# Kernel optimization log

Hardware: AMD Instinct MI355X
Metric: run time of the kernel (lower is better)

## Reference

```python
import jax, jax.numpy as jnp
import numpy as np

N_NODES = 50000
N_EDGES = 800000
IN_CH = 64
OUT_CH = 64


def setup_inputs() -> dict:
    key = jax.random.key(0)
    ks = jax.random.split(key, 20)
    inp = {
        'x': jax.random.normal(ks[0], (N_NODES, IN_CH), dtype=jnp.float32),
        'edge_index': jax.random.randint(ks[1], (2, N_EDGES), 0, N_NODES, dtype=jnp.int64),
        'edge_weight': jax.random.uniform(ks[2], (N_EDGES,), dtype=jnp.float32),
    }
    i = 3
    for g in ('z', 'r', 'h'):
        inp[f'Wx_{g}'] = 0.1 * jax.random.normal(ks[i], (2, IN_CH, OUT_CH), dtype=jnp.float32); i += 1
        inp[f'bx_{g}'] = 0.1 * jax.random.normal(ks[i], (OUT_CH,), dtype=jnp.float32); i += 1
        inp[f'Wh_{g}'] = 0.1 * jax.random.normal(ks[i], (2, OUT_CH, OUT_CH), dtype=jnp.float32); i += 1
        inp[f'bh_{g}'] = 0.1 * jax.random.normal(ks[i], (OUT_CH,), dtype=jnp.float32); i += 1
    inp['lin_W'] = 0.1 * jax.random.normal(ks[i], (OUT_CH, 1), dtype=jnp.float32); i += 1
    inp['lin_b'] = jnp.zeros((1,), dtype=jnp.float32)
    return inp


def _cheb_norm(edge_index, edge_weight, n_nodes):
    # sym-normalized scaled Laplacian with lambda_max=2: L_hat = -D^{-1/2} A D^{-1/2}
    src, dst = edge_index[0], edge_index[1]
    deg = jax.ops.segment_sum(edge_weight, src, num_segments=n_nodes)
    dinv = jnp.where(deg > 0, jax.lax.rsqrt(jnp.where(deg > 0, deg, 1.0)), 0.0)
    norm = -dinv[src] * edge_weight * dinv[dst]
    return src, dst, norm


def _cheb_conv(x, src, dst, norm, W, b, n_nodes):
    # K=2: out = x @ W0 + (L_hat x) @ W1 + b
    out = x @ W[0]
    tx1 = jax.ops.segment_sum(norm[:, None] * x[src], dst, num_segments=n_nodes)
    out = out + tx1 @ W[1]
    return out + b


def reference(x, edge_index, edge_weight,
              Wx_z, bx_z, Wh_z, bh_z,
              Wx_r, bx_r, Wh_r, bh_r,
              Wx_h, bx_h, Wh_h, bh_h,
              lin_W, lin_b):
    n = x.shape[0]
    src, dst, norm = _cheb_norm(edge_index, edge_weight, n)
    H = jnp.zeros((n, OUT_CH), dtype=x.dtype)  # GConvGRU initial hidden state
    Z = jax.nn.sigmoid(_cheb_conv(x, src, dst, norm, Wx_z, bx_z, n)
                       + _cheb_conv(H, src, dst, norm, Wh_z, bh_z, n))
    R = jax.nn.sigmoid(_cheb_conv(x, src, dst, norm, Wx_r, bx_r, n)
                       + _cheb_conv(H, src, dst, norm, Wh_r, bh_r, n))
    H_tilde = jnp.tanh(_cheb_conv(x, src, dst, norm, Wx_h, bx_h, n)
                       + _cheb_conv(H * R, src, dst, norm, Wh_h, bh_h, n))
    H = Z * H + (1.0 - Z) * H_tilde
    h = jax.nn.relu(H)
    return h @ lin_W + lin_b
```

## Files before the change

### kernel.cpp

```cpp
#include <hip/hip_runtime.h>
#include <hip/hip_bf16.h>

#define NN 50000
#define NE 800000
#define NB 196
#define BCAPD 4608
#define BCAPS 4608
#define EPT 4
#define BIN_BLOCKS ((NE + 256*EPT - 1) / (256*EPT))

typedef __attribute__((ext_vector_type(4))) float f4;
typedef __attribute__((ext_vector_type(4))) float f32x4;
typedef __attribute__((ext_vector_type(8))) short bf16x8;
typedef __attribute__((ext_vector_type(4))) unsigned int u32x4;
typedef __attribute__((ext_vector_type(2))) unsigned int u32x2;

#define OFF_TX1  0
#define OFF_BIND 0
#define OFF_BINS (NB*BCAPD*2)
#define OFF_DINV (OFF_BINS + NB*BCAPS)
#define OFF_CNT  (OFF_DINV + NN)
#define OFF_GC   (OFF_CNT + NN)
#define OFF_BIAS (OFF_GC + 2*NB)
#define OFF_WT   (OFF_BIAS + 196)
#define OFF_XB   (OFF_WT + 8192)
#define OFF_EREC (OFF_XB + NN*32)

__device__ __forceinline__ unsigned int bpack(float a, float b) {
    return ((__float_as_uint(a) + 0x8000u) >> 16)
         | ((__float_as_uint(b) + 0x8000u) & 0xffff0000u);
}

__global__ __launch_bounds__(256) void k_prep(const float* __restrict__ x,
                       const float* __restrict__ Wxz, const float* __restrict__ bxz,
                       const float* __restrict__ bhz,
                       const float* __restrict__ Wxh, const float* __restrict__ bxh,
                       const float* __restrict__ bhh,
                       const float* __restrict__ linW, const float* __restrict__ linb,
                       float* __restrict__ bias, unsigned short* __restrict__ wt,
                       unsigned int* __restrict__ xb, int* __restrict__ gc) {
    int idx = blockIdx.x * 256 + threadIdx.x;
    if (idx < NN * 16) {
        f4 v = *(const f4*)&x[(size_t)idx * 4];
        u32x2 p = { bpack(v[0], v[1]), bpack(v[2], v[3]) };
        *(u32x2*)&xb[(size_t)idx * 2] = p;
    }
    if (idx < 2 * 64 * 128) {
        int g = idx >> 13;
        int c = (idx >> 7) & 63;
        int k = idx & 127;
        const float* W = g ? Wxh : Wxz;
        float v = (k < 64) ? W[k * 64 + c] : W[4096 + (k - 64) * 64 + c];
        wt[idx] = (unsigned short)((__float_as_uint(v) + 0x8000u) >> 16);
    }
    if (idx < 64) {
        bias[idx]       = bxz[idx] + bhz[idx];
        bias[64 + idx]  = bxh[idx] + bhh[idx];
        bias[128 + idx] = linW[idx];
    }
    if (idx == 64) bias[192] = linb[0];
    if (idx < 2 * NB) gc[idx] = 0;
}

__global__ __launch_bounds__(256) void k_bin(const int* __restrict__ ei,
                                             const float* __restrict__ ew,
                                             int2* __restrict__ binD,
                                             unsigned int* __restrict__ binS,
                                             int* __restrict__ gcD, int* __restrict__ gcS) {
    __shared__ int hD[NB], hS[NB], bD[NB], bS[NB];
    int t = threadIdx.x;
    for (int b = t; b < NB; b += 256) { hD[b] = 0; hS[b] = 0; }
    __syncthreads();

    int e0 = blockIdx.x * (256 * EPT);
    unsigned int sa[EPT];
    float wv[EPT];
    int sd[EPT], ss[EPT];
#pragma unroll
    for (int i = 0; i < EPT; i++) {
        int e = e0 + i * 256 + t;
        sd[i] = -1; ss[i] = -1; sa[i] = 0; wv[i] = 0.f;
        if (e < NE) {
            int s = ei[e];
            int d = ei[NE + e];
            wv[i] = ew[e];
            int bind = d >> 8;
            sa[i] = (unsigned int)s | ((unsigned int)(d & 255) << 16)
                  | ((unsigned int)bind << 24);
            sd[i] = atomicAdd(&hD[bind], 1);
            ss[i] = atomicAdd(&hS[s >> 8], 1);
        }
    }
    __syncthreads();
    for (int b = t; b < NB; b += 256) {
        bD[b] = atomicAdd(&gcD[b], hD[b]);
        bS[b] = atomicAdd(&gcS[b], hS[b]);
    }
    __syncthreads();
#pragma unroll
    for (int i = 0; i < EPT; i++) {
        if (sd[i] < 0) continue;
        unsigned int a = sa[i];
        int bind = a >> 24;
        int src  = a & 0xffff;
        int pD = bD[bind] + sd[i];
        if (pD < BCAPD)
            binD[bind * BCAPD + pD] = make_int2((int)(a & 0xffffff), __float_as_int(wv[i]));
        int bins = src >> 8;
        int pS = bS[bins] + ss[i];
        if (pS < BCAPS)
            binS[bins * BCAPS + pS] = ((unsigned int)(src & 255) << 16)
                                    | ((__float_as_uint(wv[i]) + 0x8000u) >> 16);
    }
}

__global__ __launch_bounds__(1024) void k_split(const int2* __restrict__ binD,
                                                const unsigned int* __restrict__ binS,
                                                const int* __restrict__ gc,
                                                unsigned int* __restrict__ erec, int cap,
                                                int* __restrict__ cnt,
                                                float* __restrict__ dinv) {
    __shared__ unsigned int sh[256];
    int t = threadIdx.x;
    if (blockIdx.x < NB) {
        int bin = blockIdx.x;
        int* lcnt = (int*)sh;
        if (t < 256) lcnt[t] = 0;
        __syncthreads();
        int m = gc[bin]; if (m > BCAPD) m = BCAPD;
        const int2* bp = binD + (size_t)bin * BCAPD;
        for (int j = t; j < m; j += 1024) {
            int2 r = bp[j];
            int dlo = (r.x >> 16) & 255;
            int src = r.x & 0xffff;
            int slot = atomicAdd(&lcnt[dlo], 1);
            if (slot < cap) {
                unsigned int wr = (__float_as_uint(__int_as_float(r.y)) + 0x8000u) >> 16;
                erec[(size_t)(bin * 256 + dlo) * cap + slot] = ((unsigned int)src << 16) | wr;
            }
        }
        __syncthreads();
        if (t < 256) {
            int idx = bin * 256 + t;
            if (idx < NN) cnt[idx] = lcnt[t];
        }
    } else {
        int bin = blockIdx.x - NB;
        float* acc = (float*)sh;
        if (t < 256) acc[t] = 0.f;
        __syncthreads();
        int m = gc[NB + bin]; if (m > BCAPS) m = BCAPS;
        const unsigned int* bp = binS + (size_t)bin * BCAPS;
        for (int j = t; j < m; j += 1024) {
            unsigned int r = bp[j];
            atomicAdd(&acc[r >> 16], __uint_as_float((r & 0xffffu) << 16));
        }
        __syncthreads();
        if (t < 256) {
            int idx = bin * 256 + t;
            if (idx < NN) {
                float d = acc[t];
                dinv[idx] = (d > 0.f) ? (1.f / sqrtf(d)) : 0.f;
            }
        }
    }
}

__global__ __launch_bounds__(256) void k_gather(const unsigned int* __restrict__ xb,
                                                const int* __restrict__ cnt,
                                                const float* __restrict__ dinv,
                                                const unsigned int* __restrict__ erec,
                                                int cap, unsigned int* __restrict__ tx1) {
    int w = (blockIdx.x * 256 + threadIdx.x) >> 6;
    if (w >= NN) return;
    int lane = threadIdx.x & 63;
    int g  = lane >> 3;
    int c8 = (lane & 7) * 4;
    int kn = cnt[w];
    if (kn > cap) kn = cap;
    const unsigned int* bp = erec + (size_t)w * cap;

    f4 p0 = {0.f,0.f,0.f,0.f}, p1 = {0.f,0.f,0.f,0.f};
    f4 q0 = {0.f,0.f,0.f,0.f}, q1 = {0.f,0.f,0.f,0.f};
    int j = 0;
    for (; j + 15 < kn; j += 16) {
        unsigned int r0 = bp[j + g];
        unsigned int r1 = bp[j + 8 + g];
        int s0 = r0 >> 16, s1 = r1 >> 16;
        float n0 = dinv[s0] * __uint_as_float((r0 & 0xffffu) << 16);
        float n1 = dinv[s1] * __uint_as_float((r1 & 0xffffu) << 16);
        u32x4 v0 = *(const u32x4*)&xb[(size_t)s0 * 32 + c8];
        u32x4 v1 = *(const u32x4*)&xb[(size_t)s1 * 32 + c8];
#pragma unroll
        for (int q = 0; q < 2; q++) {
            p0[2*q]   = fmaf(n0, __uint_as_float(v0[q] << 16), p0[2*q]);
            p0[2*q+1] = fmaf(n0, __uint_as_float(v0[q] & 0xffff0000u), p0[2*q+1]);
            p1[2*q]   = fmaf(n0, __uint_as_float(v0[2+q] << 16), p1[2*q]);
            p1[2*q+1] = fmaf(n0, __uint_as_float(v0[2+q] & 0xffff0000u), p1[2*q+1]);
            q0[2*q]   = fmaf(n1, __uint_as_float(v1[q] << 16), q0[2*q]);
            q0[2*q+1] = fmaf(n1, __uint_as_float(v1[q] & 0xffff0000u), q0[2*q+1]);
            q1[2*q]   = fmaf(n1, __uint_as_float(v1[2+q] << 16), q1[2*q]);
            q1[2*q+1] = fmaf(n1, __uint_as_float(v1[2+q] & 0xffff0000u), q1[2*q+1]);
        }
    }
    for (; j + 7 < kn; j += 8) {
        unsigned int r0 = bp[j + g];
        int s0 = r0 >> 16;
        float n0 = dinv[s0] * __uint_as_float((r0 & 0xffffu) << 16);
        u32x4 v0 = *(const u32x4*)&xb[(size_t)s0 * 32 + c8];
#pragma unroll
        for (int q = 0; q < 2; q++) {
            p0[2*q]   = fmaf(n0, __uint_as_float(v0[q] << 16), p0[2*q]);
            p0[2*q+1] = fmaf(n0, __uint_as_float(v0[q] & 0xffff0000u), p0[2*q+1]);
            p1[2*q]   = fmaf(n0, __uint_as_float(v0[2+q] << 16), p1[2*q]);
            p1[2*q+1] = fmaf(n0, __uint_as_float(v0[2+q] & 0xffff0000u), p1[2*q+1]);
        }
    }
    int rem = kn - j;
    if (g < rem) {
        unsigned int r0 = bp[j + g];
        int s0 = r0 >> 16;
        float n0 = dinv[s0] * __uint_as_float((r0 & 0xffffu) << 16);
        u32x4 v0 = *(const u32x4*)&xb[(size_t)s0 * 32 + c8];
#pragma unroll
        for (int q = 0; q < 2; q++) {
            p0[2*q]   = fmaf(n0, __uint_as_float(v0[q] << 16), p0[2*q]);
            p0[2*q+1] = fmaf(n0, __uint_as_float(v0[q] & 0xffff0000u), p0[2*q+1]);
            p1[2*q]   = fmaf(n0, __uint_as_float(v0[2+q] << 16), p1[2*q]);
            p1[2*q+1] = fmaf(n0, __uint_as_float(v0[2+q] & 0xffff0000u), p1[2*q+1]);
        }
    }
    p0 += q0; p1 += q1;
#pragma unroll
    for (int q = 0; q < 4; q++) {
        p0[q] += __shfl_xor(p0[q], 8);  p1[q] += __shfl_xor(p1[q], 8);
        p0[q] += __shfl_xor(p0[q], 16); p1[q] += __shfl_xor(p1[q], 16);
        p0[q] += __shfl_xor(p0[q], 32); p1[q] += __shfl_xor(p1[q], 32);
    }
    if (g == 0) {
        float nd = -dinv[w];
        u32x4 o = { bpack(nd*p0[0], nd*p0[1]), bpack(nd*p0[2], nd*p0[3]),
                    bpack(nd*p1[0], nd*p1[1]), bpack(nd*p1[2], nd*p1[3]) };
        *(u32x4*)&tx1[(size_t)w * 32 + c8] = o;
    }
}

__global__ __launch_bounds__(256) void k_node(const unsigned int* __restrict__ xb,
                                              const unsigned int* __restrict__ tx1,
                                              const unsigned short* __restrict__ WT,
                                              const float* __restrict__ bias,
                                              float* __restrict__ out) {
    int lane = threadIdx.x & 63;
    int base = (blockIdx.x * 4 + (threadIdx.x >> 6)) * 16;
    if (base >= NN) return;

    int m  = lane & 15;
    int kg = lane >> 4;
    size_t node = (size_t)(base + m);

    bf16x8 afr[4];
    afr[0] = *(const bf16x8*)&xb[node * 32 + kg * 4];
    afr[1] = *(const bf16x8*)&xb[node * 32 + 16 + kg * 4];
    afr[2] = *(const bf16x8*)&tx1[node * 32 + kg * 4];
    afr[3] = *(const bf16x8*)&tx1[node * 32 + 16 + kg * 4];

    const unsigned short* Wl = WT + m * 128 + kg * 8;
    f32x4 az4[4], ah4[4];
#pragma unroll
    for (int nt = 0; nt < 4; nt++) { az4[nt] = (f32x4){0,0,0,0}; ah4[nt] = (f32x4){0,0,0,0}; }

#pragma unroll
    for (int nt = 0; nt < 4; nt++) {
#pragma unroll
        for (int kt = 0; kt < 4; kt++) {
            bf16x8 bz = *(const bf16x8*)(Wl + nt * 2048 + kt * 32);
            bf16x8 bh = *(const bf16x8*)(Wl + 8192 + nt * 2048 + kt * 32);
            az4[nt] = __builtin_amdgcn_mfma_f32_16x16x32_bf16(afr[kt], bz, az4[nt], 0, 0, 0);
            ah4[nt] = __builtin_amdgcn_mfma_f32_16x16x32_bf16(afr[kt], bh, ah4[nt], 0, 0, 0);
        }
    }

    float vout[4] = {0.f, 0.f, 0.f, 0.f};
#pragma unroll
    for (int nt = 0; nt < 4; nt++) {
        int col = nt * 16 + m;
        float bz = bias[col], bh = bias[64 + col], lw = bias[128 + col];
#pragma unroll
        for (int r = 0; r < 4; r++) {
            float az = az4[nt][r] + bz;
            float ah = ah4[nt][r] + bh;
            float ez = __expf(-az);
            float z  = __builtin_amdgcn_rcpf(1.f + ez);
            float eh = __expf(2.f * ah);
            float th = (eh - 1.f) * __builtin_amdgcn_rcpf(eh + 1.f);
            float h  = (1.f - z) * th;
            h = (h > 0.f) ? h : 0.f;
            vout[r] = fmaf(h, lw, vout[r]);
        }
    }
    float LB = bias[192];
#pragma unroll
    for (int r = 0; r < 4; r++) {
        float v = vout[r];
        v += __shfl_xor(v, 1);
        v += __shfl_xor(v, 2);
        v += __shfl_xor(v, 4);
        v += __shfl_xor(v, 8);
        if (m == 0) out[base + kg * 4 + r] = v + LB;
    }
}

extern "C" void kernel_launch(void* const* d_in, const int* in_sizes, int n_in,
                              void* d_out, int out_size, void* d_ws, size_t ws_size,
                              hipStream_t stream) {
    const float* x   = (const float*)d_in[0];
    const int*   ei  = (const int*)d_in[1];
    const float* ew  = (const float*)d_in[2];
    const float* Wxz = (const float*)d_in[3];
    const float* bxz = (const float*)d_in[4];
    const float* bhz = (const float*)d_in[6];
    const float* Wxh = (const float*)d_in[11];
    const float* bxh = (const float*)d_in[12];
    const float* bhh = (const float*)d_in[14];
    const float* lW  = (const float*)d_in[15];
    const float* lb  = (const float*)d_in[16];
    float* ws  = (float*)d_ws;
    float* out = (float*)d_out;

    long long availInts = (long long)(ws_size / 4) - (long long)OFF_EREC;
    int cap = 64;
    if (availInts < (long long)NN * 64) cap = 56;
    if (availInts < (long long)NN * 56) cap = 48;
    if (availInts < (long long)NN * 48) cap = 32;
    unsigned int* erec = (unsigned int*)(ws + OFF_EREC);

    k_prep<<<(NN * 16 + 255) / 256, 256, 0, stream>>>(
        x, Wxz, bxz, bhz, Wxh, bxh, bhh, lW, lb,
        ws + OFF_BIAS, (unsigned short*)(ws + OFF_WT),
        (unsigned int*)(ws + OFF_XB), (int*)(ws + OFF_GC));
    k_bin<<<BIN_BLOCKS, 256, 0, stream>>>(ei, ew,
                                          (int2*)(ws + OFF_BIND),
                                          (unsigned int*)(ws + OFF_BINS),
                                          (int*)(ws + OFF_GC), (int*)(ws + OFF_GC) + NB);
    k_split<<<2 * NB, 1024, 0, stream>>>((const int2*)(ws + OFF_BIND),
                                         (const unsigned int*)(ws + OFF_BINS),
                                         (const int*)(ws + OFF_GC), erec, cap,
                                         (int*)(ws + OFF_CNT), ws + OFF_DINV);
    k_gather<<<(NN * 64 + 255) / 256, 256, 0, stream>>>(
        (const unsigned int*)(ws + OFF_XB), (const int*)(ws + OFF_CNT),
        ws + OFF_DINV, erec, cap, (unsigned int*)(ws + OFF_TX1));
    k_node<<<(NN + 63) / 64, 256, 0, stream>>>(
        (const unsigned int*)(ws + OFF_XB), (const unsigned int*)(ws + OFF_TX1),
        (const unsigned short*)(ws + OFF_WT), ws + OFF_BIAS, out);
}
```

Before: 99.59 us.

## Precompute full edge norm in bucketing and merge prep with binning kernel

The degree computation is split into its own kernel so the bucketing pass can fold the full symmetric norm (-dinv[src]*w*dinv[dst]) into each edge record as bf16. The gather kernel then no longer does random dinv lookups per edge or the final per-node scaling. Separately, the x/weight prep kernel is merged into the binning kernel via block-index dispatch, and the counter reset moves to a memset. The launch count stays the same, with an extra dependency stage (deg before bucket), and quantizing the combined norm to bf16 changes rounding slightly.

```diff
diff --git a/kernel.cpp b/kernel.cpp
--- a/kernel.cpp
+++ b/kernel.cpp
@@ -8,6 +8,7 @@
 #define BCAPS 4608
 #define EPT 4
 #define BIN_BLOCKS ((NE + 256*EPT - 1) / (256*EPT))
+#define PREP_BLOCKS ((NN*16 + 255) / 256)
 
 typedef __attribute__((ext_vector_type(4))) float f4;
 typedef __attribute__((ext_vector_type(4))) float f32x4;
@@ -31,144 +32,148 @@
          | ((__float_as_uint(b) + 0x8000u) & 0xffff0000u);
 }
 
-__global__ __launch_bounds__(256) void k_prep(const float* __restrict__ x,
-                       const float* __restrict__ Wxz, const float* __restrict__ bxz,
-                       const float* __restrict__ bhz,
-                       const float* __restrict__ Wxh, const float* __restrict__ bxh,
-                       const float* __restrict__ bhh,
-                       const float* __restrict__ linW, const float* __restrict__ linb,
-                       float* __restrict__ bias, unsigned short* __restrict__ wt,
-                       unsigned int* __restrict__ xb, int* __restrict__ gc) {
-    int idx = blockIdx.x * 256 + threadIdx.x;
-    if (idx < NN * 16) {
-        f4 v = *(const f4*)&x[(size_t)idx * 4];
-        u32x2 p = { bpack(v[0], v[1]), bpack(v[2], v[3]) };
-        *(u32x2*)&xb[(size_t)idx * 2] = p;
-    }
-    if (idx < 2 * 64 * 128) {
-        int g = idx >> 13;
-        int c = (idx >> 7) & 63;
-        int k = idx & 127;
-        const float* W = g ? Wxh : Wxz;
-        float v = (k < 64) ? W[k * 64 + c] : W[4096 + (k - 64) * 64 + c];
-        wt[idx] = (unsigned short)((__float_as_uint(v) + 0x8000u) >> 16);
-    }
-    if (idx < 64) {
-        bias[idx]       = bxz[idx] + bhz[idx];
-        bias[64 + idx]  = bxh[idx] + bhh[idx];
-        bias[128 + idx] = linW[idx];
-    }
-    if (idx == 64) bias[192] = linb[0];
-    if (idx < 2 * NB) gc[idx] = 0;
-}
-
-__global__ __launch_bounds__(256) void k_bin(const int* __restrict__ ei,
-                                             const float* __restrict__ ew,
-                                             int2* __restrict__ binD,
-                                             unsigned int* __restrict__ binS,
-                                             int* __restrict__ gcD, int* __restrict__ gcS) {
+__global__ __launch_bounds__(256) void k_prepbin(
+        const int* __restrict__ ei, const float* __restrict__ ew,
+        const float* __restrict__ x,
+        const float* __restrict__ Wxz, const float* __restrict__ bxz,
+        const float* __restrict__ bhz,
+        const float* __restrict__ Wxh, const float* __restrict__ bxh,
+        const float* __restrict__ bhh,
+        const float* __restrict__ linW, const float* __restrict__ linb,
+        int2* __restrict__ binD, unsigned int* __restrict__ binS,
+        int* __restrict__ gcD, int* __restrict__ gcS,
+        float* __restrict__ bias, unsigned short* __restrict__ wt,
+        unsigned int* __restrict__ xb) {
     __shared__ int hD[NB], hS[NB], bD[NB], bS[NB];
     int t = threadIdx.x;
-    for (int b = t; b < NB; b += 256) { hD[b] = 0; hS[b] = 0; }
+    if (blockIdx.x < BIN_BLOCKS) {
+        for (int b = t; b < NB; b += 256) { hD[b] = 0; hS[b] = 0; }
+        __syncthreads();
+        int e0 = blockIdx.x * (256 * EPT);
+        unsigned int sa[EPT];
+        float wv[EPT];
+        int sd[EPT], ss[EPT];
+#pragma unroll
+        for (int i = 0; i < EPT; i++) {
+            int e = e0 + i * 256 + t;
+            sd[i] = -1; ss[i] = -1; sa[i] = 0; wv[i] = 0.f;
+            if (e < NE) {
+                int s = ei[e];
+                int d = ei[NE + e];
+                wv[i] = ew[e];
+                int bind = d >> 8;
+                sa[i] = (unsigned int)s | ((unsigned int)(d & 255) << 16)
+                      | ((unsigned int)bind << 24);
+                sd[i] = atomicAdd(&hD[bind], 1);
+                ss[i] = atomicAdd(&hS[s >> 8], 1);
+            }
+        }
+        __syncthreads();
+        for (int b = t; b < NB; b += 256) {
+            bD[b] = atomicAdd(&gcD[b], hD[b]);
+            bS[b] = atomicAdd(&gcS[b], hS[b]);
+        }
+        __syncthreads();
+#pragma unroll
+        for (int i = 0; i < EPT; i++) {
+            if (sd[i] < 0) continue;
+            unsigned int a = sa[i];
+            int bind = a >> 24;
+            int src  = a & 0xffff;
+            int pD = bD[bind] + sd[i];
+            if (pD < BCAPD)
+                binD[bind * BCAPD + pD] = make_int2((int)(a & 0xffffff),
+                                                    __float_as_int(wv[i]));
+            int bins = src >> 8;
+            int pS = bS[bins] + ss[i];
+            if (pS < BCAPS)
+                binS[bins * BCAPS + pS] = ((unsigned int)(src & 255) << 16)
+                                        | ((__float_as_uint(wv[i]) + 0x8000u) >> 16);
+        }
+    } else {
+        int idx = (blockIdx.x - BIN_BLOCKS) * 256 + t;
+        if (idx < NN * 16) {
+            f4 v = *(const f4*)&x[(size_t)idx * 4];
+            u32x2 p = { bpack(v[0], v[1]), bpack(v[2], v[3]) };
+            *(u32x2*)&xb[(size_t)idx * 2] = p;
+        }
+        if (idx < 2 * 64 * 128) {
+            int g = idx >> 13;
+            int c = (idx >> 7) & 63;
+            int k = idx & 127;
+            const float* W = g ? Wxh : Wxz;
+            float v = (k < 64) ? W[k * 64 + c] : W[4096 + (k - 64) * 64 + c];
+            wt[idx] = (unsigned short)((__float_as_uint(v) + 0x8000u) >> 16);
+        }
+        if (idx < 64) {
+            bias[idx]       = bxz[idx] + bhz[idx];
+            bias[64 + idx]  = bxh[idx] + bhh[idx];
+            bias[128 + idx] = linW[idx];
+        }
+        if (idx == 64) bias[192] = linb[0];
+    }
+}
+
+__global__ __launch_bounds__(1024) void k_deg(const unsigned int* __restrict__ binS,
+                                              const int* __restrict__ gcS,
+                                              float* __restrict__ dinv) {
+    __shared__ float acc[256];
+    int bin = blockIdx.x;
+    int t = threadIdx.x;
+    if (t < 256) acc[t] = 0.f;
     __syncthreads();
-
-    int e0 = blockIdx.x * (256 * EPT);
-    unsigned int sa[EPT];
-    float wv[EPT];
-    int sd[EPT], ss[EPT];
-#pragma unroll
-    for (int i = 0; i < EPT; i++) {
-        int e = e0 + i * 256 + t;
-        sd[i] = -1; ss[i] = -1; sa[i] = 0; wv[i] = 0.f;
-        if (e < NE) {
-            int s = ei[e];
-            int d = ei[NE + e];
-            wv[i] = ew[e];
-            int bind = d >> 8;
-            sa[i] = (unsigned int)s | ((unsigned int)(d & 255) << 16)
-                  | ((unsigned int)bind << 24);
-            sd[i] = atomicAdd(&hD[bind], 1);
-            ss[i] = atomicAdd(&hS[s >> 8], 1);
-        }
+    int m = gcS[bin]; if (m > BCAPS) m = BCAPS;
+    const unsigned int* bp = binS + (size_t)bin * BCAPS;
+    for (int j = t; j < m; j += 1024) {
+        unsigned int r = bp[j];
+        atomicAdd(&acc[r >> 16], __uint_as_float((r & 0xffffu) << 16));
     }
     __syncthreads();
-    for (int b = t; b < NB; b += 256) {
-        bD[b] = atomicAdd(&gcD[b], hD[b]);
-        bS[b] = atomicAdd(&gcS[b], hS[b]);
+    if (t < 256) {
+        int idx = bin * 256 + t;
+        if (idx < NN) {
+            float d = acc[t];
+            dinv[idx] = (d > 0.f) ? (1.f / sqrtf(d)) : 0.f;
+        }
+    }
+}
+
+__global__ __launch_bounds__(1024) void k_bucket(const int2* __restrict__ binD,
+                                                 const int* __restrict__ gcD,
+                                                 const float* __restrict__ dinv,
+                                                 unsigned int* __restrict__ erec, int cap,
+                                                 int* __restrict__ cnt) {
+    __shared__ int lcnt[256];
+    __shared__ float ddv[256];
+    int bin = blockIdx.x;
+    int t = threadIdx.x;
+    if (t < 256) {
+        lcnt[t] = 0;
+        int idx = bin * 256 + t;
+        ddv[t] = (idx < NN) ? dinv[idx] : 0.f;
     }
     __syncthreads();
-#pragma unroll
-    for (int i = 0; i < EPT; i++) {
-        if (sd[i] < 0) continue;
-        unsigned int a = sa[i];
-        int bind = a >> 24;
-        int src  = a & 0xffff;
-        int pD = bD[bind] + sd[i];
-        if (pD < BCAPD)
-            binD[bind * BCAPD + pD] = make_int2((int)(a & 0xffffff), __float_as_int(wv[i]));
-        int bins = src >> 8;
-        int pS = bS[bins] + ss[i];
-        if (pS < BCAPS)
-            binS[bins * BCAPS + pS] = ((unsigned int)(src & 255) << 16)
-                                    | ((__float_as_uint(wv[i]) + 0x8000u) >> 16);
-    }
-}
-
-__global__ __launch_bounds__(1024) void k_split(const int2* __restrict__ binD,
-                                                const unsigned int* __restrict__ binS,
-                                                const int* __restrict__ gc,
-                                                unsigned int* __restrict__ erec, int cap,
-                                                int* __restrict__ cnt,
-                                                float* __restrict__ dinv) {
-    __shared__ unsigned int sh[256];
-    int t = threadIdx.x;
-    if (blockIdx.x < NB) {
-        int bin = blockIdx.x;
-        int* lcnt = (int*)sh;
-        if (t < 256) lcnt[t] = 0;
-        __syncthreads();
-        int m = gc[bin]; if (m > BCAPD) m = BCAPD;
-        const int2* bp = binD + (size_t)bin * BCAPD;
-        for (int j = t; j < m; j += 1024) {
-            int2 r = bp[j];
-            int dlo = (r.x >> 16) & 255;
-            int src = r.x & 0xffff;
-            int slot = atomicAdd(&lcnt[dlo], 1);
-            if (slot < cap) {
-                unsigned int wr = (__float_as_uint(__int_as_float(r.y)) + 0x8000u) >> 16;
-                erec[(size_t)(bin * 256 + dlo) * cap + slot] = ((unsigned int)src << 16) | wr;
-            }
-        }
-        __syncthreads();
-        if (t < 256) {
-            int idx = bin * 256 + t;
-            if (idx < NN) cnt[idx] = lcnt[t];
-        }
-    } else {
-        int bin = blockIdx.x - NB;
-        float* acc = (float*)sh;
-        if (t < 256) acc[t] = 0.f;
-        __syncthreads();
-        int m = gc[NB + bin]; if (m > BCAPS) m = BCAPS;
-        const unsigned int* bp = binS + (size_t)bin * BCAPS;
-        for (int j = t; j < m; j += 1024) {
-            unsigned int r = bp[j];
-            atomicAdd(&acc[r >> 16], __uint_as_float((r & 0xffffu) << 16));
-        }
-        __syncthreads();
-        if (t < 256) {
-            int idx = bin * 256 + t;
-            if (idx < NN) {
-                float d = acc[t];
-                dinv[idx] = (d > 0.f) ? (1.f / sqrtf(d)) : 0.f;
-            }
-        }
+    int m = gcD[bin]; if (m > BCAPD) m = BCAPD;
+    const int2* bp = binD + (size_t)bin * BCAPD;
+    for (int j = t; j < m; j += 1024) {
+        int2 r = bp[j];
+        int dlo = (r.x >> 16) & 255;
+        int src = r.x & 0xffff;
+        float nrm = -dinv[src] * __int_as_float(r.y) * ddv[dlo];
+        int slot = atomicAdd(&lcnt[dlo], 1);
+        if (slot < cap)
+            erec[(size_t)(bin * 256 + dlo) * cap + slot] =
+                ((unsigned int)src << 16) | ((__float_as_uint(nrm) + 0x8000u) >> 16);
+    }
+    __syncthreads();
+    if (t < 256) {
+        int idx = bin * 256 + t;
+        if (idx < NN) cnt[idx] = lcnt[t];
     }
 }
 
 __global__ __launch_bounds__(256) void k_gather(const unsigned int* __restrict__ xb,
                                                 const int* __restrict__ cnt,
-                                                const float* __restrict__ dinv,
                                                 const unsigned int* __restrict__ erec,
                                                 int cap, unsigned int* __restrict__ tx1) {
     int w = (blockIdx.x * 256 + threadIdx.x) >> 6;
@@ -186,11 +191,10 @@
     for (; j + 15 < kn; j += 16) {
         unsigned int r0 = bp[j + g];
         unsigned int r1 = bp[j + 8 + g];
-        int s0 = r0 >> 16, s1 = r1 >> 16;
-        float n0 = dinv[s0] * __uint_as_float((r0 & 0xffffu) << 16);
-        float n1 = dinv[s1] * __uint_as_float((r1 & 0xffffu) << 16);
-        u32x4 v0 = *(const u32x4*)&xb[(size_t)s0 * 32 + c8];
-        u32x4 v1 = *(const u32x4*)&xb[(size_t)s1 * 32 + c8];
+        float n0 = __uint_as_float(r0 << 16);
+        float n1 = __uint_as_float(r1 << 16);
+        u32x4 v0 = *(const u32x4*)&xb[(size_t)(r0 >> 16) * 32 + c8];
+        u32x4 v1 = *(const u32x4*)&xb[(size_t)(r1 >> 16) * 32 + c8];
 #pragma unroll
         for (int q = 0; q < 2; q++) {
             p0[2*q]   = fmaf(n0, __uint_as_float(v0[q] << 16), p0[2*q]);
@@ -205,9 +209,8 @@
     }
     for (; j + 7 < kn; j += 8) {
         unsigned int r0 = bp[j + g];
-        int s0 = r0 >> 16;
-        float n0 = dinv[s0] * __uint_as_float((r0 & 0xffffu) << 16);
-        u32x4 v0 = *(const u32x4*)&xb[(size_t)s0 * 32 + c8];
+        float n0 = __uint_as_float(r0 << 16);
+        u32x4 v0 = *(const u32x4*)&xb[(size_t)(r0 >> 16) * 32 + c8];
 #pragma unroll
         for (int q = 0; q < 2; q++) {
             p0[2*q]   = fmaf(n0, __uint_as_float(v0[q] << 16), p0[2*q]);
@@ -219,9 +222,8 @@
     int rem = kn - j;
     if (g < rem) {
         unsigned int r0 = bp[j + g];
-        int s0 = r0 >> 16;
-        float n0 = dinv[s0] * __uint_as_float((r0 & 0xffffu) << 16);
-        u32x4 v0 = *(const u32x4*)&xb[(size_t)s0 * 32 + c8];
+        float n0 = __uint_as_float(r0 << 16);
+        u32x4 v0 = *(const u32x4*)&xb[(size_t)(r0 >> 16) * 32 + c8];
 #pragma unroll
         for (int q = 0; q < 2; q++) {
             p0[2*q]   = fmaf(n0, __uint_as_float(v0[q] << 16), p0[2*q]);
@@ -238,9 +240,8 @@
         p0[q] += __shfl_xor(p0[q], 32); p1[q] += __shfl_xor(p1[q], 32);
     }
     if (g == 0) {
-        float nd = -dinv[w];
-        u32x4 o = { bpack(nd*p0[0], nd*p0[1]), bpack(nd*p0[2], nd*p0[3]),
-                    bpack(nd*p1[0], nd*p1[1]), bpack(nd*p1[2], nd*p1[3]) };
+        u32x4 o = { bpack(p0[0], p0[1]), bpack(p0[2], p0[3]),
+                    bpack(p1[0], p1[1]), bpack(p1[2], p1[3]) };
         *(u32x4*)&tx1[(size_t)w * 32 + c8] = o;
     }
 }
@@ -334,21 +335,21 @@
     if (availInts < (long long)NN * 48) cap = 32;
     unsigned int* erec = (unsigned int*)(ws + OFF_EREC);
 
-    k_prep<<<(NN * 16 + 255) / 256, 256, 0, stream>>>(
-        x, Wxz, bxz, bhz, Wxh, bxh, bhh, lW, lb,
+    hipMemsetAsync(ws + OFF_GC, 0, 2 * NB * sizeof(int), stream);
+    k_prepbin<<<BIN_BLOCKS + PREP_BLOCKS, 256, 0, stream>>>(
+        ei, ew, x, Wxz, bxz, bhz, Wxh, bxh, bhh, lW, lb,
+        (int2*)(ws + OFF_BIND), (unsigned int*)(ws + OFF_BINS),
+        (int*)(ws + OFF_GC), (int*)(ws + OFF_GC) + NB,
         ws + OFF_BIAS, (unsigned short*)(ws + OFF_WT),
-        (unsigned int*)(ws + OFF_XB), (int*)(ws + OFF_GC));
-    k_bin<<<BIN_BLOCKS, 256, 0, stream>>>(ei, ew,
-                                          (int2*)(ws + OFF_BIND),
-                                          (unsigned int*)(ws + OFF_BINS),
-                                          (int*)(ws + OFF_GC), (int*)(ws + OFF_GC) + NB);
-    k_split<<<2 * NB, 1024, 0, stream>>>((const int2*)(ws + OFF_BIND),
-                                         (const unsigned int*)(ws + OFF_BINS),
-                                         (const int*)(ws + OFF_GC), erec, cap,
-                                         (int*)(ws + OFF_CNT), ws + OFF_DINV);
+        (unsigned int*)(ws + OFF_XB));
+    k_deg<<<NB, 1024, 0, stream>>>((const unsigned int*)(ws + OFF_BINS),
+                                   (const int*)(ws + OFF_GC) + NB, ws + OFF_DINV);
+    k_bucket<<<NB, 1024, 0, stream>>>((const int2*)(ws + OFF_BIND),
+                                      (const int*)(ws + OFF_GC), ws + OFF_DINV,
+                                      erec, cap, (int*)(ws + OFF_CNT));
     k_gather<<<(NN * 64 + 255) / 256, 256, 0, stream>>>(
         (const unsigned int*)(ws + OFF_XB), (const int*)(ws + OFF_CNT),
-        ws + OFF_DINV, erec, cap, (unsigned int*)(ws + OFF_TX1));
+        erec, cap, (unsigned int*)(ws + OFF_TX1));
     k_node<<<(NN + 63) / 64, 256, 0, stream>>>(
         (const unsigned int*)(ws + OFF_XB), (const unsigned int*)(ws + OFF_TX1),
         (const unsigned short*)(ws + OFF_WT), ws + OFF_BIAS, out);
```

New measurement: 107.0 us. +7.5%, slower.
